# Optimization experiments

Measured on AMD Instinct MI355X. Metric: run time of the kernel, lower is better.

The kernel has to match this reference:

```python
import jax, jax.numpy as jnp
import numpy as np

B, M, D, H = 2, 2048, 1024, 16
DH = D // H            # 64 head dim
R_ATTN = 512           # rank of q/k/v SVD factors
FFN_D = 2048           # GEGLU inner dim; Wi out = 2*FFN_D
R_FFN = 1024           # rank of FFN SVD factors
ROPE_BASE = 10000.0
LN_EPS = 1e-5


def _layernorm(x, g, b):
    mu = jnp.mean(x, axis=-1, keepdims=True)
    var = jnp.mean(jnp.square(x - mu), axis=-1, keepdims=True)
    return (x - mu) * jax.lax.rsqrt(var + LN_EPS) * g + b


def _rotate_half(x):
    x1, x2 = jnp.split(x, 2, axis=-1)
    return jnp.concatenate((-x2, x1), axis=-1)


def _rope_cos_sin(m, dh, dtype):
    inv_freq = 1.0 / (ROPE_BASE ** (jnp.arange(0, dh, 2, dtype=jnp.float32) / dh))
    freqs = jnp.arange(m, dtype=jnp.float32)[:, None] * inv_freq[None, :]  # [M, dh/2]
    emb = jnp.concatenate((freqs, freqs), axis=-1)  # [M, dh]
    return jnp.cos(emb).astype(dtype), jnp.sin(emb).astype(dtype)


def setup_inputs() -> dict:
    key = jax.random.key(0)
    ks = iter(jax.random.split(key, 32))
    rn = lambda shape, s: jax.random.normal(next(ks), shape, jnp.float32) * s
    w = 0.02
    return {
        'hidden_states': rn((B, M, D), 1.0),
        'ln1_g': jnp.ones((D,), jnp.float32), 'ln1_b': jnp.zeros((D,), jnp.float32),
        'Uq': rn((D, R_ATTN), w), 'Vq': rn((R_ATTN, D), w), 'bq': rn((D,), w),
        'Uk': rn((D, R_ATTN), w), 'Vk': rn((R_ATTN, D), w), 'bk': rn((D,), w),
        'Uv': rn((D, R_ATTN), w), 'Vv': rn((R_ATTN, D), w), 'bv': rn((D,), w),
        'Wo': rn((D, D), w), 'bo': rn((D,), w),  # dense attn out proj, torch [out,in]
        'ln2_g': jnp.ones((D,), jnp.float32), 'ln2_b': jnp.zeros((D,), jnp.float32),
        'U1': rn((D, R_FFN), w), 'V1': rn((R_FFN, 2 * FFN_D), w), 'b1': rn((2 * FFN_D,), w),
        'U2': rn((FFN_D, R_FFN), w), 'V2': rn((R_FFN, D), w), 'b2': rn((D,), w),
    }


def reference(hidden_states, ln1_g, ln1_b, Uq, Vq, bq, Uk, Vk, bk, Uv, Vv, bv,
              Wo, bo, ln2_g, ln2_b, U1, V1, b1, U2, V2, b2):
    x = hidden_states
    xn = _layernorm(x, ln1_g, ln1_b)
    # low-rank QKV: y = (x @ U) @ V + b
    q = (xn @ Uq) @ Vq + bq
    k = (xn @ Uk) @ Vk + bk
    v = (xn @ Uv) @ Vv + bv
    to_bhmd = lambda t: t.reshape(B, M, H, DH).transpose(0, 2, 1, 3)
    q, k, v = to_bhmd(q), to_bhmd(k), to_bhmd(v)
    cos, sin = _rope_cos_sin(M, DH, q.dtype)  # [M, DH]
    q = q * cos + _rotate_half(q) * sin
    k = k * cos + _rotate_half(k) * sin
    scale = 1.0 / np.sqrt(DH)
    scores = jnp.einsum('bhmd,bhnd->bhmn', q, k) * scale  # [B,H,M,M]
    attn = jax.nn.softmax(scores, axis=-1)
    out = jnp.einsum('bhmn,bhnd->bhmd', attn, v)
    out = out.transpose(0, 2, 1, 3).reshape(B, M, D)
    x = x + out @ Wo.T + bo
    # low-rank GEGLU FFN
    xn2 = _layernorm(x, ln2_g, ln2_b)
    z = (xn2 @ U1) @ V1 + b1  # [B,M,2*FFN_D]
    z1, z2 = jnp.split(z, 2, axis=-1)
    h = jax.nn.gelu(z1, approximate=True) * z2  # GEGLU, tanh approx
    y = (h @ U2) @ V2 + b2
    return x + y
```

## Files before the change

kernel.cpp:

```cpp
#include <hip/hip_runtime.h>


typedef unsigned short u16;
typedef unsigned int u32;
typedef u16 u16x8 __attribute__((ext_vector_type(8)));
typedef __bf16 bf16x8 __attribute__((ext_vector_type(8)));
typedef float f32x4 __attribute__((ext_vector_type(4)));

__device__ __forceinline__ u16 f2bf(float f) {
    u32 u = __builtin_bit_cast(u32, f);
    u += 0x7fff + ((u >> 16) & 1);
    return (u16)(u >> 16);
}
__device__ __forceinline__ u16 f2bf_t(float f) {
    return (u16)(__builtin_bit_cast(u32, f) >> 16);
}
__device__ __forceinline__ float bf2f(u16 h) {
    u32 u = ((u32)h) << 16;
    return __builtin_bit_cast(float, u);
}

__device__ __forceinline__ void gload16(const void* g, void* l) {
    __builtin_amdgcn_global_load_lds(
        (const __attribute__((address_space(1))) void*)g,
        (__attribute__((address_space(3))) void*)l, 16, 0, 0);
}

template <int CTRL>
__device__ __forceinline__ float dppror(float x) {
    return __builtin_bit_cast(float,
        __builtin_amdgcn_mov_dpp(__builtin_bit_cast(int, x), CTRL, 0xF, 0xF, true));
}
__device__ __forceinline__ float rowsum16(float x) {
    x += dppror<0x128>(x);
    x += dppror<0x124>(x);
    x += dppror<0x122>(x);
    x += dppror<0x121>(x);
    return x;
}

#define MB 1048576u
#define OFF_UQKVT (0*MB)
#define OFF_VQKVT (3*MB)
#define OFF_WOB   (6*MB)
#define OFF_U1T   (8*MB)
#define OFF_V1TP  (10*MB)
#define OFF_U2T   (18*MB)
#define OFF_V2T   (22*MB)
#define OFF_BQKV  (24*MB)
#define OFF_B1P   (24*MB + 16384u)
#define OFF_XN    (25*MB)
#define OFF_TBUF  (33*MB)
#define OFF_QB    (45*MB)
#define OFF_KB    (53*MB)
#define OFF_HB    (45*MB)
#define OFF_VTB   (61*MB)
#define OFF_OB    (69*MB)
#define OFF_X2    (93*MB)

__global__ __launch_bounds__(256) void prep_kernel(
    const float* __restrict__ Uq, const float* __restrict__ Uk,
    const float* __restrict__ Uv, const float* __restrict__ Vq,
    const float* __restrict__ Vk, const float* __restrict__ Vv,
    const float* __restrict__ Wo, const float* __restrict__ U1,
    const float* __restrict__ V1, const float* __restrict__ U2,
    const float* __restrict__ V2,
    const float* __restrict__ bq, const float* __restrict__ bk,
    const float* __restrict__ bv, const float* __restrict__ b1,
    u16* __restrict__ UQKVT, u16* __restrict__ VQKVT, u16* __restrict__ WOB,
    u16* __restrict__ U1T, u16* __restrict__ V1TP, u16* __restrict__ U2T,
    u16* __restrict__ V2T, float* __restrict__ BQKV, float* __restrict__ B1P)
{
    __shared__ float tile[32][33];
    int bid = blockIdx.x;

    if (bid >= 12288) {
        int id = (bid - 12288) * 256 + threadIdx.x;
        if (id < 3072) {
            float v = (id < 1024) ? bq[id] : (id < 2048 ? bk[id - 1024] : bv[id - 2048]);
            BQKV[id] = v;
        }
        int g = id >> 5, s = id & 31;
        B1P[id] = b1[(s < 16) ? (g*16 + s) : (2048 + g*16 + (s - 16))];
        return;
    }
    if (bid >= 11264) {
        int i4 = ((bid - 11264) * 256 + threadIdx.x) * 4;
        float4 v = *(const float4*)(Wo + i4);
        u16 tmp[4] = {f2bf(v.x), f2bf(v.y), f2bf(v.z), f2bf(v.w)};
        *(uint2*)(WOB + i4) = *(const uint2*)tmp;
        return;
    }

    const float* src; u16* dst; int K, N, src_ld, nx; bool gg = false;
    if (bid < 3072) {
        int t = bid / 512; bid -= t * 512;
        if (t < 3) { src = t==0 ? Uq : (t==1 ? Uk : Uv);
                     dst = UQKVT + t * 512*1024; K = 1024; N = 512; src_ld = 512; nx = 16; }
        else { int z = t - 3; src = z==0 ? Vq : (z==1 ? Vk : Vv);
               dst = VQKVT + z * 524288; K = 512; N = 1024; src_ld = 1024; nx = 32; }
    } else if (bid < 4096)  { src = U1; dst = U1T;  K = 1024; N = 1024; src_ld = 1024; nx = 32;  bid -= 3072; }
    else if (bid < 8192)    { src = V1; dst = V1TP; K = 1024; N = 4096; src_ld = 4096; nx = 128; bid -= 4096; gg = true; }
    else if (bid < 10240)   { src = U2; dst = U2T;  K = 2048; N = 1024; src_ld = 1024; nx = 32;  bid -= 8192; }
    else                    { src = V2; dst = V2T;  K = 1024; N = 1024; src_ld = 1024; nx = 32;  bid -= 10240; }

    int tx = threadIdx.x & 31, ty = threadIdx.x >> 5;
    int n0 = (bid % nx) * 32, k0 = (bid / nx) * 32;
    int srccol;
    if (gg) { int g = n0 >> 5; srccol = (tx < 16) ? (g*16 + tx) : (2048 + g*16 + (tx - 16)); }
    else srccol = n0 + tx;
    for (int i = 0; i < 4; i++)
        tile[ty + i*8][tx] = src[(size_t)(k0 + ty + i*8) * src_ld + srccol];
    __syncthreads();
    for (int i = 0; i < 4; i++)
        dst[(size_t)(n0 + ty + i*8) * K + k0 + tx] = f2bf(tile[tx][ty + i*8]);
}

__global__ __launch_bounds__(256) void ln_kernel(
    const float* __restrict__ x, const float* __restrict__ g,
    const float* __restrict__ bta, u16* __restrict__ out)
{
    int w = threadIdx.x >> 6, lane = threadIdx.x & 63;
    int row = blockIdx.x * 4 + w;
    const float* xr = x + (size_t)row * 1024;
    float vals[16];
    float s = 0.f, s2 = 0.f;
    #pragma unroll
    for (int ii = 0; ii < 16; ii++) {
        float v = xr[lane + ii*64];
        vals[ii] = v; s += v; s2 += v * v;
    }
    #pragma unroll
    for (int off = 1; off < 64; off <<= 1) {
        s  += __shfl_xor(s, off);
        s2 += __shfl_xor(s2, off);
    }
    float mu = s * (1.f/1024.f);
    float var = s2 * (1.f/1024.f) - mu * mu;
    float rs = rsqrtf(var + 1e-5f);
    #pragma unroll
    for (int ii = 0; ii < 16; ii++) {
        int col = lane + ii*64;
        out[(size_t)row * 1024 + col] = f2bf((vals[ii] - mu) * rs * g[col] + bta[col]);
    }
}

__global__ __launch_bounds__(256) void gemm_bt_kernel(
    const u16* __restrict__ A, int lda, const u16* __restrict__ Bt,
    void* __restrict__ Cout, int ldc, const float* __restrict__ bias,
    const float* __restrict__ resid, int Kdim, int mode)
{
    __shared__ u16 As[2][4096];
    __shared__ u16 Bs[2][4096];
    int tid = threadIdx.x;
    int m0 = blockIdx.y * 128, n0 = blockIdx.x * 128;
    int w = tid >> 6, lane = tid & 63, quad = lane >> 4, l15 = lane & 15;
    int wm = (w >> 1) * 64, wn = (w & 1) * 64;
    int sr = tid >> 2, sc8 = (tid & 3) * 8;

    f32x4 acc[4][4] = {};

    const u16* Ap = A  + (size_t)(m0 + sr) * lda  + sc8;
    const u16* Bp = Bt + (size_t)(n0 + sr) * Kdim + sc8;

    #define GSTAGE(buf, koff) do {                                        \
        gload16(Ap + (koff),                     &As[buf][tid * 8]);      \
        gload16(Ap + (koff) + (size_t)64 * lda,  &As[buf][2048 + tid*8]); \
        gload16(Bp + (koff),                     &Bs[buf][tid * 8]);      \
        gload16(Bp + (koff) + (size_t)64 * Kdim, &Bs[buf][2048 + tid*8]); \
    } while (0)

    GSTAGE(0, 0);
    __syncthreads();

    for (int k0 = 0; k0 < Kdim; k0 += 32) {
        int cur = (k0 >> 5) & 1;
        if (k0 + 32 < Kdim) GSTAGE(cur ^ 1, k0 + 32);
        const u16* Asc = As[cur];
        const u16* Bsc = Bs[cur];
        bf16x8 af[4], bfr[4];
        #pragma unroll
        for (int i = 0; i < 4; i++)
            af[i] = *(const bf16x8*)&Asc[(wm + i*16 + l15) * 32 + quad * 8];
        #pragma unroll
        for (int j = 0; j < 4; j++)
            bfr[j] = *(const bf16x8*)&Bsc[(wn + j*16 + l15) * 32 + quad * 8];
        #pragma unroll
        for (int i = 0; i < 4; i++)
            #pragma unroll
            for (int j = 0; j < 4; j++)
                acc[i][j] = __builtin_amdgcn_mfma_f32_16x16x32_bf16(af[i], bfr[j], acc[i][j], 0, 0, 0);
        __syncthreads();
    }
    #undef GSTAGE

    if (mode == 2) {
        u16* hb = (u16*)Cout;
        #pragma unroll
        for (int i = 0; i < 4; i++) {
            int row = m0 + wm + i*16 + quad*4;
            #pragma unroll
            for (int p = 0; p < 2; p++) {
                int colz = n0 + wn + p*32 + l15;
                float bz1 = bias[colz], bz2 = bias[colz + 16];
                int hcol = ((n0 + wn) >> 1) + p*16 + l15;
                #pragma unroll
                for (int r = 0; r < 4; r++) {
                    float z1 = acc[i][2*p][r] + bz1;
                    float z2 = acc[i][2*p+1][r] + bz2;
                    float uu = 0.7978845608028654f * (z1 + 0.044715f * z1 * z1 * z1);
                    float e = __expf(2.f * uu);
                    float th = (e - 1.f) / (e + 1.f);
                    float hv = 0.5f * z1 * (1.f + th) * z2;
                    hb[(size_t)(row + r) * ldc + hcol] = f2bf(hv);
                }
            }
        }
        return;
    }
    #pragma unroll
    for (int i = 0; i < 4; i++) {
        int row = m0 + wm + i*16 + quad*4;
        #pragma unroll
        for (int j = 0; j < 4; j++) {
            int col = n0 + wn + j*16 + l15;
            float bv = bias ? bias[col] : 0.f;
            #pragma unroll
            for (int r = 0; r < 4; r++) {
                float v = acc[i][j][r] + bv;
                size_t idx = (size_t)(row + r) * ldc + col;
                if (mode == 0) ((float*)Cout)[idx] = v + resid[idx];
                else           ((u16*)Cout)[idx] = f2bf(v);
            }
        }
    }
}

__global__ __launch_bounds__(256) void qkv2_kernel(
    const u16* __restrict__ T, const u16* __restrict__ Vw,
    const float* __restrict__ bqkv, u16* __restrict__ qout,
    u16* __restrict__ kout, u16* __restrict__ vtout)
{
    __shared__ u16 As[2][4096];
    __shared__ u16 Bs[2][4096];
    int tid = threadIdx.x;
    int z = blockIdx.z;
    int m0 = blockIdx.y * 128, n0 = blockIdx.x * 128;
    int w = tid >> 6, lane = tid & 63, quad = lane >> 4, l15 = lane & 15;
    int wm = (w >> 1) * 64, wn = (w & 1) * 64;
    int sr = tid >> 2, sc8 = (tid & 3) * 8;

    f32x4 acc[4][4] = {};

    const u16* Ap = T  + (size_t)z * 512 + (size_t)(m0 + sr) * 1536 + sc8;
    const u16* Bp = Vw + (size_t)z * 512 * 1024 + (size_t)(n0 + sr) * 512 + sc8;

    #define QSTAGE(buf, koff) do {                                        \
        gload16(Ap + (koff),                     &As[buf][tid * 8]);      \
        gload16(Ap + (koff) + (size_t)64 * 1536, &As[buf][2048 + tid*8]); \
        gload16(Bp + (koff),                     &Bs[buf][tid * 8]);      \
        gload16(Bp + (koff) + (size_t)64 * 512,  &Bs[buf][2048 + tid*8]); \
    } while (0)

    QSTAGE(0, 0);
    __syncthreads();

    for (int k0 = 0; k0 < 512; k0 += 32) {
        int cur = (k0 >> 5) & 1;
        if (k0 + 32 < 512) QSTAGE(cur ^ 1, k0 + 32);
        const u16* Asc = As[cur];
        const u16* Bsc = Bs[cur];
        bf16x8 af[4], bfr[4];
        #pragma unroll
        for (int i = 0; i < 4; i++)
            af[i] = *(const bf16x8*)&Asc[(wm + i*16 + l15) * 32 + quad * 8];
        #pragma unroll
        for (int j = 0; j < 4; j++)
            bfr[j] = *(const bf16x8*)&Bsc[(wn + j*16 + l15) * 32 + quad * 8];
        #pragma unroll
        for (int i = 0; i < 4; i++)
            #pragma unroll
            for (int j = 0; j < 4; j++)
                acc[i][j] = __builtin_amdgcn_mfma_f32_16x16x32_bf16(af[i], bfr[j], acc[i][j], 0, 0, 0);
        __syncthreads();
    }
    #undef QSTAGE

    const float* bias = bqkv + z * 1024;
    if (z < 2) {
        u16* Ob = z ? kout : qout;
        float qscale = z ? 1.f : 0.18033688011112042f;
        #pragma unroll
        for (int i = 0; i < 4; i++) {
            int row0 = m0 + wm + i*16 + quad*4;
            #pragma unroll
            for (int j = 0; j < 2; j++) {
                int col = n0 + wn + j*16 + l15;
                float bj = bias[col], bj2 = bias[col + 32];
                float invf = exp2f((float)(col & 31) * -0.4152410118609203f);
                #pragma unroll
                for (int r = 0; r < 4; r++) {
                    int t = row0 + r;
                    float fr = (float)(t & 2047) * invf;
                    float sn, cs;
                    __sincosf(fr, &sn, &cs);
                    sn *= qscale; cs *= qscale;
                    float v1 = acc[i][j][r] + bj;
                    float v2 = acc[i][j+2][r] + bj2;
                    Ob[(size_t)t * 1024 + col]      = f2bf(v1 * cs - v2 * sn);
                    Ob[(size_t)t * 1024 + col + 32] = f2bf(v2 * cs + v1 * sn);
                }
            }
        }
    } else {
        int bb = m0 >> 11;
        #pragma unroll
        for (int i = 0; i < 4; i++) {
            int row0 = m0 + wm + i*16 + quad*4;
            #pragma unroll
            for (int j = 0; j < 4; j++) {
                int col = n0 + wn + j*16 + l15;
                float bj = bias[col];
                u16 pack[4];
                #pragma unroll
                for (int r = 0; r < 4; r++) pack[r] = f2bf(acc[i][j][r] + bj);
                size_t dst = ((size_t)(bb * 16 + (col >> 6)) * 64 + (col & 63)) * 2048 + (row0 & 2047);
                *(uint2*)&vtout[dst] = *(const uint2*)pack;
            }
        }
    }
}

__global__ __launch_bounds__(256) void attn_kernel(
    const u16* __restrict__ Q, const u16* __restrict__ K,
    const u16* __restrict__ Vt, u16* __restrict__ O)
{
    __shared__ u16 Ks[2][64 * 64];
    __shared__ u16 Vs[2][64 * 64];
    __shared__ u16 Ps[128 * 72];
    int tid = threadIdx.x;
    int bh = blockIdx.x;
    int b = bh >> 4, h = bh & 15;
    int m0 = blockIdx.y * 128;
    int w = tid >> 6, lane = tid & 63, quad = lane >> 4, l15 = lane & 15;
    int wm = w * 32;
    size_t qkbase = (size_t)b * 2048 * 1024 + h * 64;
    const u16* Vg = Vt + (size_t)bh * 64 * 2048;

    bf16x8 qf[2][2];
    #pragma unroll
    for (int i = 0; i < 2; i++)
        #pragma unroll
        for (int ks = 0; ks < 2; ks++)
            qf[i][ks] = *(const bf16x8*)(Q + qkbase +
                (size_t)(m0 + wm + i*16 + l15) * 1024 + ks*32 + quad*8);

    f32x4 oacc[2][4] = {};
    float lsum[2][4] = {};

    int r0 = tid >> 3, p = tid & 7;
    int c0 = (p ^ (r0 & 7)) * 8;
    int xsw = l15 & 7;

    #define STAGE(buf, key0) do {                                               \
        gload16(K + qkbase + (size_t)((key0) + r0) * 1024 + c0,                 \
                &Ks[buf][r0 * 64 + p * 8]);                                     \
        gload16(K + qkbase + (size_t)((key0) + r0 + 32) * 1024 + c0,            \
                &Ks[buf][(r0 + 32) * 64 + p * 8]);                              \
        gload16(Vg + (size_t)r0 * 2048 + (key0) + c0,                           \
                &Vs[buf][r0 * 64 + p * 8]);                                     \
        gload16(Vg + (size_t)(r0 + 32) * 2048 + (key0) + c0,                    \
                &Vs[buf][(r0 + 32) * 64 + p * 8]);                              \
    } while (0)

    STAGE(0, 0);
    __syncthreads();

    for (int kt = 0; kt < 32; kt++) {
        int cur = kt & 1;
        if (kt < 31) STAGE(cur ^ 1, (kt + 1) * 64);
        const u16* Ksc = Ks[cur];
        const u16* Vsc = Vs[cur];

        f32x4 sacc[2][4] = {};
        #pragma unroll
        for (int ks = 0; ks < 2; ks++) {
            bf16x8 kf[4];
            #pragma unroll
            for (int j = 0; j < 4; j++)
                kf[j] = *(const bf16x8*)&Ksc[(j*16 + l15) * 64 + (((ks*4 + quad) ^ xsw) * 8)];
            #pragma unroll
            for (int i = 0; i < 2; i++)
                #pragma unroll
                for (int j = 0; j < 4; j++)
                    sacc[i][j] = __builtin_amdgcn_mfma_f32_16x16x32_bf16(qf[i][ks], kf[j], sacc[i][j], 0, 0, 0);
        }

        #pragma unroll
        for (int i = 0; i < 2; i++) {
            int prow0 = (wm + i*16 + quad*4) * 72;
            #pragma unroll
            for (int r = 0; r < 4; r++) {
                float p0 = __builtin_amdgcn_exp2f(sacc[i][0][r]);
                float p1 = __builtin_amdgcn_exp2f(sacc[i][1][r]);
                float p2 = __builtin_amdgcn_exp2f(sacc[i][2][r]);
                float p3 = __builtin_amdgcn_exp2f(sacc[i][3][r]);
                lsum[i][r] += (p0 + p1) + (p2 + p3);
                int pr = prow0 + r * 72;
                Ps[pr + l15]      = f2bf_t(p0);
                Ps[pr + 16 + l15] = f2bf_t(p1);
                Ps[pr + 32 + l15] = f2bf_t(p2);
                Ps[pr + 48 + l15] = f2bf_t(p3);
            }
        }

        #pragma unroll
        for (int ks = 0; ks < 2; ks++) {
            bf16x8 pf[2], vf[4];
            #pragma unroll
            for (int i = 0; i < 2; i++)
                pf[i] = *(const bf16x8*)&Ps[(wm + i*16 + l15) * 72 + ks*32 + quad*8];
            #pragma unroll
            for (int j = 0; j < 4; j++)
                vf[j] = *(const bf16x8*)&Vsc[(j*16 + l15) * 64 + (((ks*4 + quad) ^ xsw) * 8)];
            #pragma unroll
            for (int i = 0; i < 2; i++)
                #pragma unroll
                for (int j = 0; j < 4; j++)
                    oacc[i][j] = __builtin_amdgcn_mfma_f32_16x16x32_bf16(pf[i], vf[j], oacc[i][j], 0, 0, 0);
        }
        __syncthreads();
    }
    #undef STAGE

    #pragma unroll
    for (int i = 0; i < 2; i++)
        #pragma unroll
        for (int r = 0; r < 4; r++) {
            float inv = 1.f / rowsum16(lsum[i][r]);
            int row = m0 + wm + i*16 + quad*4 + r;
            #pragma unroll
            for (int j = 0; j < 4; j++)
                O[qkbase + (size_t)row * 1024 + j*16 + l15] = f2bf(oacc[i][j][r] * inv);
        }
}

extern "C" void kernel_launch(void* const* d_in, const int* in_sizes, int n_in,
                              void* d_out, int out_size, void* d_ws, size_t ws_size,
                              hipStream_t stream) {
    (void)in_sizes; (void)n_in; (void)out_size; (void)ws_size;
    const float* x     = (const float*)d_in[0];
    const float* ln1_g = (const float*)d_in[1];
    const float* ln1_b = (const float*)d_in[2];
    const float* Uq    = (const float*)d_in[3];
    const float* Vq    = (const float*)d_in[4];
    const float* bq    = (const float*)d_in[5];
    const float* Uk    = (const float*)d_in[6];
    const float* Vk    = (const float*)d_in[7];
    const float* bk    = (const float*)d_in[8];
    const float* Uv    = (const float*)d_in[9];
    const float* Vv    = (const float*)d_in[10];
    const float* bv    = (const float*)d_in[11];
    const float* Wo    = (const float*)d_in[12];
    const float* bo    = (const float*)d_in[13];
    const float* ln2_g = (const float*)d_in[14];
    const float* ln2_b = (const float*)d_in[15];
    const float* U1    = (const float*)d_in[16];
    const float* V1    = (const float*)d_in[17];
    const float* b1    = (const float*)d_in[18];
    const float* U2    = (const float*)d_in[19];
    const float* V2    = (const float*)d_in[20];
    const float* b2    = (const float*)d_in[21];
    float* out = (float*)d_out;
    char* ws = (char*)d_ws;

    u16* UQKVT = (u16*)(ws + OFF_UQKVT);
    u16* VQKVT = (u16*)(ws + OFF_VQKVT);
    u16* WOB   = (u16*)(ws + OFF_WOB);
    u16* U1T   = (u16*)(ws + OFF_U1T);
    u16* V1TP  = (u16*)(ws + OFF_V1TP);
    u16* U2T   = (u16*)(ws + OFF_U2T);
    u16* V2T   = (u16*)(ws + OFF_V2T);
    float* BQKV = (float*)(ws + OFF_BQKV);
    float* B1P  = (float*)(ws + OFF_B1P);
    u16* xn  = (u16*)(ws + OFF_XN);
    u16* tbuf= (u16*)(ws + OFF_TBUF);
    u16* qb  = (u16*)(ws + OFF_QB);
    u16* kb  = (u16*)(ws + OFF_KB);
    u16* vtb = (u16*)(ws + OFF_VTB);
    u16* ob  = (u16*)(ws + OFF_OB);
    u16* hb  = (u16*)(ws + OFF_HB);
    float* x2 = (float*)(ws + OFF_X2);

    prep_kernel<<<12304, 256, 0, stream>>>(
        Uq, Uk, Uv, Vq, Vk, Vv, Wo, U1, V1, U2, V2, bq, bk, bv, b1,
        UQKVT, VQKVT, WOB, U1T, V1TP, U2T, V2T, BQKV, B1P);

    ln_kernel<<<1024, 256, 0, stream>>>(x, ln1_g, ln1_b, xn);

    gemm_bt_kernel<<<dim3(12, 32), 256, 0, stream>>>(xn, 1024, UQKVT, tbuf, 1536,
                                                     nullptr, nullptr, 1024, 1);
    qkv2_kernel<<<dim3(8, 32, 3), 256, 0, stream>>>(tbuf, VQKVT, BQKV, qb, kb, vtb);

    attn_kernel<<<dim3(32, 16), 256, 0, stream>>>(qb, kb, vtb, ob);

    gemm_bt_kernel<<<dim3(8, 32), 256, 0, stream>>>(ob, 1024, WOB, x2, 1024,
                                                    bo, x, 1024, 0);
    ln_kernel<<<1024, 256, 0, stream>>>(x2, ln2_g, ln2_b, xn);

    gemm_bt_kernel<<<dim3(8, 32), 256, 0, stream>>>(xn, 1024, U1T, tbuf, 1024,
                                                    nullptr, nullptr, 1024, 1);
    gemm_bt_kernel<<<dim3(32, 32), 256, 0, stream>>>(tbuf, 1024, V1TP, hb, 2048,
                                                     B1P, nullptr, 1024, 2);
    gemm_bt_kernel<<<dim3(8, 32), 256, 0, stream>>>(hb, 2048, U2T, tbuf, 1024,
                                                    nullptr, nullptr, 2048, 1);
    gemm_bt_kernel<<<dim3(8, 32), 256, 0, stream>>>(tbuf, 1024, V2T, out, 1024,
                                                    b2, x2, 1024, 0);
}
```

Measured before the change: 468.9 us.

## Add 128x64-tile GEMM for small-N projections and transpose attention score MFMA

Adds a GEMM variant with 128x64 output tiles and uses it for the QKV-down, Wo, U1, U2 and V2 projections. This doubles the block count so the 256 CUs are better filled on these small-N matmuls, at the cost of lower per-block data reuse. In attention, the QK^T MFMA operands are swapped so each lane holds four consecutive keys of one query row. P can then be packed and stored as 8-byte writes, and the row sum reduces to two cross-lane shuffles instead of per-element DPP reductions.

```diff
diff --git a/kernel.cpp b/kernel.cpp
--- a/kernel.cpp
+++ b/kernel.cpp
@@ -12,31 +12,19 @@
     u += 0x7fff + ((u >> 16) & 1);
     return (u16)(u >> 16);
 }
-__device__ __forceinline__ u16 f2bf_t(float f) {
-    return (u16)(__builtin_bit_cast(u32, f) >> 16);
-}
 __device__ __forceinline__ float bf2f(u16 h) {
     u32 u = ((u32)h) << 16;
     return __builtin_bit_cast(float, u);
+}
+__device__ __forceinline__ u32 packbf(float a, float b) {
+    return __builtin_amdgcn_perm(__builtin_bit_cast(u32, b),
+                                 __builtin_bit_cast(u32, a), 0x07060302u);
 }
 
 __device__ __forceinline__ void gload16(const void* g, void* l) {
     __builtin_amdgcn_global_load_lds(
         (const __attribute__((address_space(1))) void*)g,
         (__attribute__((address_space(3))) void*)l, 16, 0, 0);
-}
-
-template <int CTRL>
-__device__ __forceinline__ float dppror(float x) {
-    return __builtin_bit_cast(float,
-        __builtin_amdgcn_mov_dpp(__builtin_bit_cast(int, x), CTRL, 0xF, 0xF, true));
-}
-__device__ __forceinline__ float rowsum16(float x) {
-    x += dppror<0x128>(x);
-    x += dppror<0x124>(x);
-    x += dppror<0x122>(x);
-    x += dppror<0x121>(x);
-    return x;
 }
 
 #define MB 1048576u
@@ -236,6 +224,72 @@
     }
 }
 
+__global__ __launch_bounds__(256) void gemm_bt64_kernel(
+    const u16* __restrict__ A, int lda, const u16* __restrict__ Bt,
+    void* __restrict__ Cout, int ldc, const float* __restrict__ bias,
+    const float* __restrict__ resid, int Kdim, int mode)
+{
+    __shared__ u16 As[2][4096];
+    __shared__ u16 Bs[2][2048];
+    int tid = threadIdx.x;
+    int m0 = blockIdx.y * 128, n0 = blockIdx.x * 64;
+    int w = tid >> 6, lane = tid & 63, quad = lane >> 4, l15 = lane & 15;
+    int wm = (w >> 1) * 64, wn = (w & 1) * 32;
+    int sr = tid >> 2, sc8 = (tid & 3) * 8;
+
+    f32x4 acc[4][2] = {};
+
+    const u16* Ap = A  + (size_t)(m0 + sr) * lda  + sc8;
+    const u16* Bp = Bt + (size_t)(n0 + sr) * Kdim + sc8;
+
+    #define GSTAGE64(buf, koff) do {                                       \
+        gload16(Ap + (koff),                     &As[buf][tid * 8]);       \
+        gload16(Ap + (koff) + (size_t)64 * lda,  &As[buf][2048 + tid*8]);  \
+        gload16(Bp + (koff),                     &Bs[buf][tid * 8]);       \
+    } while (0)
+
+    GSTAGE64(0, 0);
+    __syncthreads();
+
+    for (int k0 = 0; k0 < Kdim; k0 += 32) {
+        int cur = (k0 >> 5) & 1;
+        if (k0 + 32 < Kdim) GSTAGE64(cur ^ 1, k0 + 32);
+        const u16* Asc = As[cur];
+        const u16* Bsc = Bs[cur];
+        bf16x8 af[4], bfr[2];
+        #pragma unroll
+        for (int i = 0; i < 4; i++)
+            af[i] = *(const bf16x8*)&Asc[(wm + i*16 + l15) * 32 + quad * 8];
+        #pragma unroll
+        for (int j = 0; j < 2; j++)
+            bfr[j] = *(const bf16x8*)&Bsc[(wn + j*16 + l15) * 32 + quad * 8];
+        #pragma unroll
+        for (int i = 0; i < 4; i++)
+            #pragma unroll
+            for (int j = 0; j < 2; j++)
+                acc[i][j] = __builtin_amdgcn_mfma_f32_16x16x32_bf16(af[i], bfr[j], acc[i][j], 0, 0, 0);
+        __syncthreads();
+    }
+    #undef GSTAGE64
+
+    #pragma unroll
+    for (int i = 0; i < 4; i++) {
+        int row = m0 + wm + i*16 + quad*4;
+        #pragma unroll
+        for (int j = 0; j < 2; j++) {
+            int col = n0 + wn + j*16 + l15;
+            float bv = bias ? bias[col] : 0.f;
+            #pragma unroll
+            for (int r = 0; r < 4; r++) {
+                float v = acc[i][j][r] + bv;
+                size_t idx = (size_t)(row + r) * ldc + col;
+                if (mode == 0) ((float*)Cout)[idx] = v + resid[idx];
+                else           ((u16*)Cout)[idx] = f2bf(v);
+            }
+        }
+    }
+}
+
 __global__ __launch_bounds__(256) void qkv2_kernel(
     const u16* __restrict__ T, const u16* __restrict__ Vw,
     const float* __restrict__ bqkv, u16* __restrict__ qout,
@@ -356,7 +410,7 @@
                 (size_t)(m0 + wm + i*16 + l15) * 1024 + ks*32 + quad*8);
 
     f32x4 oacc[2][4] = {};
-    float lsum[2][4] = {};
+    float lsum[2] = {};
 
     int r0 = tid >> 3, p = tid & 7;
     int c0 = (p ^ (r0 & 7)) * 8;
@@ -382,35 +436,32 @@
         const u16* Ksc = Ks[cur];
         const u16* Vsc = Vs[cur];
 
-        f32x4 sacc[2][4] = {};
+        f32x4 sacc[4][2] = {};
         #pragma unroll
         for (int ks = 0; ks < 2; ks++) {
             bf16x8 kf[4];
             #pragma unroll
-            for (int j = 0; j < 4; j++)
-                kf[j] = *(const bf16x8*)&Ksc[(j*16 + l15) * 64 + (((ks*4 + quad) ^ xsw) * 8)];
-            #pragma unroll
-            for (int i = 0; i < 2; i++)
+            for (int jj = 0; jj < 4; jj++)
+                kf[jj] = *(const bf16x8*)&Ksc[(jj*16 + l15) * 64 + (((ks*4 + quad) ^ xsw) * 8)];
+            #pragma unroll
+            for (int jj = 0; jj < 4; jj++)
                 #pragma unroll
-                for (int j = 0; j < 4; j++)
-                    sacc[i][j] = __builtin_amdgcn_mfma_f32_16x16x32_bf16(qf[i][ks], kf[j], sacc[i][j], 0, 0, 0);
+                for (int i = 0; i < 2; i++)
+                    sacc[jj][i] = __builtin_amdgcn_mfma_f32_16x16x32_bf16(kf[jj], qf[i][ks], sacc[jj][i], 0, 0, 0);
         }
 
         #pragma unroll
         for (int i = 0; i < 2; i++) {
-            int prow0 = (wm + i*16 + quad*4) * 72;
-            #pragma unroll
-            for (int r = 0; r < 4; r++) {
-                float p0 = __builtin_amdgcn_exp2f(sacc[i][0][r]);
-                float p1 = __builtin_amdgcn_exp2f(sacc[i][1][r]);
-                float p2 = __builtin_amdgcn_exp2f(sacc[i][2][r]);
-                float p3 = __builtin_amdgcn_exp2f(sacc[i][3][r]);
-                lsum[i][r] += (p0 + p1) + (p2 + p3);
-                int pr = prow0 + r * 72;
-                Ps[pr + l15]      = f2bf_t(p0);
-                Ps[pr + 16 + l15] = f2bf_t(p1);
-                Ps[pr + 32 + l15] = f2bf_t(p2);
-                Ps[pr + 48 + l15] = f2bf_t(p3);
+            int prow = (wm + i*16 + l15) * 72 + quad*4;
+            #pragma unroll
+            for (int jj = 0; jj < 4; jj++) {
+                float p0 = __builtin_amdgcn_exp2f(sacc[jj][i][0]);
+                float p1 = __builtin_amdgcn_exp2f(sacc[jj][i][1]);
+                float p2 = __builtin_amdgcn_exp2f(sacc[jj][i][2]);
+                float p3 = __builtin_amdgcn_exp2f(sacc[jj][i][3]);
+                lsum[i] += (p0 + p1) + (p2 + p3);
+                uint2 pk; pk.x = packbf(p0, p1); pk.y = packbf(p2, p3);
+                *(uint2*)&Ps[prow + jj*16] = pk;
             }
         }
 
@@ -433,15 +484,24 @@
     }
     #undef STAGE
 
+    float inv[2][4];
+    #pragma unroll
+    for (int i = 0; i < 2; i++) {
+        float s = lsum[i];
+        s += __shfl_xor(s, 16);
+        s += __shfl_xor(s, 32);
+        #pragma unroll
+        for (int r = 0; r < 4; r++)
+            inv[i][r] = 1.f / __shfl(s, (lane & 48) | (quad*4 + r));
+    }
     #pragma unroll
     for (int i = 0; i < 2; i++)
         #pragma unroll
         for (int r = 0; r < 4; r++) {
-            float inv = 1.f / rowsum16(lsum[i][r]);
             int row = m0 + wm + i*16 + quad*4 + r;
             #pragma unroll
             for (int j = 0; j < 4; j++)
-                O[qkbase + (size_t)row * 1024 + j*16 + l15] = f2bf(oacc[i][j][r] * inv);
+                O[qkbase + (size_t)row * 1024 + j*16 + l15] = f2bf(oacc[i][j][r] * inv[i][r]);
         }
 }
 
@@ -498,22 +558,22 @@
 
     ln_kernel<<<1024, 256, 0, stream>>>(x, ln1_g, ln1_b, xn);
 
-    gemm_bt_kernel<<<dim3(12, 32), 256, 0, stream>>>(xn, 1024, UQKVT, tbuf, 1536,
-                                                     nullptr, nullptr, 1024, 1);
+    gemm_bt64_kernel<<<dim3(24, 32), 256, 0, stream>>>(xn, 1024, UQKVT, tbuf, 1536,
+                                                       nullptr, nullptr, 1024, 1);
     qkv2_kernel<<<dim3(8, 32, 3), 256, 0, stream>>>(tbuf, VQKVT, BQKV, qb, kb, vtb);
 
     attn_kernel<<<dim3(32, 16), 256, 0, stream>>>(qb, kb, vtb, ob);
 
-    gemm_bt_kernel<<<dim3(8, 32), 256, 0, stream>>>(ob, 1024, WOB, x2, 1024,
-                                                    bo, x, 1024, 0);
+    gemm_bt64_kernel<<<dim3(16, 32), 256, 0, stream>>>(ob, 1024, WOB, x2, 1024,
+                                                       bo, x, 1024, 0);
     ln_kernel<<<1024, 256, 0, stream>>>(x2, ln2_g, ln2_b, xn);
 
-    gemm_bt_kernel<<<dim3(8, 32), 256, 0, stream>>>(xn, 1024, U1T, tbuf, 1024,
-                                                    nullptr, nullptr, 1024, 1);
+    gemm_bt64_kernel<<<dim3(16, 32), 256, 0, stream>>>(xn, 1024, U1T, tbuf, 1024,
+                                                       nullptr, nullptr, 1024, 1);
     gemm_bt_kernel<<<dim3(32, 32), 256, 0, stream>>>(tbuf, 1024, V1TP, hb, 2048,
                                                      B1P, nullptr, 1024, 2);
-    gemm_bt_kernel<<<dim3(8, 32), 256, 0, stream>>>(hb, 2048, U2T, tbuf, 1024,
-                                                    nullptr, nullptr, 2048, 1);
-    gemm_bt_kernel<<<dim3(8, 32), 256, 0, stream>>>(tbuf, 1024, V2T, out, 1024,
-                                                    b2, x2, 1024, 0);
-}
+    gemm_bt64_kernel<<<dim3(16, 32), 256, 0, stream>>>(hb, 2048, U2T, tbuf, 1024,
+                                                       nullptr, nullptr, 2048, 1);
+    gemm_bt64_kernel<<<dim3(16, 32), 256, 0, stream>>>(tbuf, 1024, V2T, out, 1024,
+                                                       b2, x2, 1024, 0);
+}
```

Result: faster. 426.6 us (-9.0%).
